# Performance work log

Measured on AMD Instinct MI355X. Metric: run time of the kernel, lower is better.

## Reference

```python
import jax, jax.numpy as jnp
import numpy as np

N = 20000      # total nodes across the mini-batch of graphs
E = 320000     # edges (avg degree 16)
B = 16         # graphs in the batch
HEADS = 8
EPS_BN = 1e-5
NEG_SLOPE = 0.2


def _lin(k, fan_in, fan_out):
    return (jax.random.normal(k, (fan_in, fan_out), jnp.float32) / np.float32(np.sqrt(fan_in)))


def setup_inputs() -> dict:
    key = jax.random.key(0)
    ks = jax.random.split(key, 24)
    inp = {}
    inp["x"] = jax.random.normal(ks[0], (N, 3), jnp.float32)
    inp["edge_index"] = jax.random.randint(ks[1], (2, E), 0, N, dtype=jnp.int32)
    inp["batch"] = jnp.sort(jax.random.randint(ks[2], (N,), 0, B, dtype=jnp.int32))
    # GATConv params: lin weight [in, heads*out], att_src/att_dst [heads,out], bias [heads*out]
    dims = [(3, 16), (128, 32), (256, 64)]
    for i, (cin, cout) in enumerate(dims, start=1):
        base = 3 + 5 * i
        inp[f"W{i}"] = _lin(ks[base], cin, HEADS * cout)
        inp[f"as{i}"] = jax.random.normal(ks[base + 1], (HEADS, cout), jnp.float32) * 0.1
        inp[f"ad{i}"] = jax.random.normal(ks[base + 2], (HEADS, cout), jnp.float32) * 0.1
        inp[f"b{i}"] = jnp.zeros((HEADS * cout,), jnp.float32)
        inp[f"g{i}"] = jnp.ones((HEADS * cout,), jnp.float32)
        inp[f"be{i}"] = jnp.zeros((HEADS * cout,), jnp.float32)
    inp["fcW"] = _lin(ks[20], 512, 10)
    inp["fcb"] = jnp.zeros((10,), jnp.float32)
    return inp


def gat_layer(x, src, dst, W, a_s, a_d, bias, heads, out_ch):
    n = x.shape[0]
    h = (x @ W).reshape(n, heads, out_ch)              # [N,H,C]
    al_s = jnp.einsum('nhc,hc->nh', h, a_s)            # [N,H]
    al_d = jnp.einsum('nhc,hc->nh', h, a_d)
    e = jax.nn.leaky_relu(al_s[src] + al_d[dst], NEG_SLOPE)   # [E,H]
    m = jax.ops.segment_max(e, dst, num_segments=n)    # per-dst softmax (stable)
    e = jnp.exp(e - m[dst])
    denom = jax.ops.segment_sum(e, dst, num_segments=n)
    alpha = e / (denom[dst] + 1e-16)
    out = jax.ops.segment_sum(h[src] * alpha[:, :, None], dst, num_segments=n)
    return out.reshape(n, heads * out_ch) + bias


def bn_relu(x, g, b):
    mu = x.mean(0)
    var = x.var(0)  # biased, as torch BN uses for normalization
    return jax.nn.relu((x - mu) * jax.lax.rsqrt(var + EPS_BN) * g + b)


def reference(x, edge_index, batch, W1, as1, ad1, b1, g1, be1,
              W2, as2, ad2, b2, g2, be2, W3, as3, ad3, b3, g3, be3, fcW, fcb):
    n = x.shape[0]
    loops = jnp.arange(n, dtype=edge_index.dtype)
    src = jnp.concatenate([edge_index[0], loops])  # add_self_loops=True (PyG default)
    dst = jnp.concatenate([edge_index[1], loops])
    h = bn_relu(gat_layer(x, src, dst, W1, as1, ad1, b1, HEADS, 16), g1, be1)
    h = bn_relu(gat_layer(h, src, dst, W2, as2, ad2, b2, HEADS, 32), g2, be2)
    h = bn_relu(gat_layer(h, src, dst, W3, as3, ad3, b3, HEADS, 64), g3, be3)
    pooled = jax.ops.segment_max(h, batch, num_segments=B)  # global_max_pool
    return pooled @ fcW + fcb
```

## Files before the change

### kernel.cpp

```cpp
#include <hip/hip_runtime.h>
#include <hip/hip_bf16.h>

#define HEADS 8
#define EPS_BN 1e-5f
#define NEG_SLOPE 0.2f
#define BN_NB 256

typedef __attribute__((ext_vector_type(8))) short bf16x8;
typedef __attribute__((ext_vector_type(4))) float f32x4;

__device__ __forceinline__ float bf2f(unsigned short u) {
    return __uint_as_float(((unsigned int)u) << 16);
}

__device__ __forceinline__ unsigned short f2bf(float f) {
    __hip_bfloat16 b = __float2bfloat16(f);
    return *reinterpret_cast<unsigned short*>(&b);
}

__device__ __forceinline__ void gld_lds16(const ushort* g, ushort* l) {
    __builtin_amdgcn_global_load_lds(
        (const __attribute__((address_space(1))) unsigned int*)g,
        (__attribute__((address_space(3))) unsigned int*)l, 16, 0, 0);
}


__global__ void count_kernel(const int* __restrict__ ei, int E, int N, int* __restrict__ counts) {
    int i = blockIdx.x * blockDim.x + threadIdx.x;
    int total = E + N;
    if (i >= total) return;
    int d = (i < E) ? ei[E + i] : (i - E);
    atomicAdd(&counts[d], 1);
}

__global__ __launch_bounds__(1024) void scan_block_kernel(const int* __restrict__ counts,
                                                          int* __restrict__ offs,
                                                          int* __restrict__ part, int n) {
    __shared__ int tile[1024];
    int tid = threadIdx.x;
    int gid = blockIdx.x * 1024 + tid;
    int v = (gid < n) ? counts[gid] : 0;
    tile[tid] = v;
    __syncthreads();
    for (int off = 1; off < 1024; off <<= 1) {
        int t = (tid >= off) ? tile[tid - off] : 0;
        __syncthreads();
        tile[tid] += t;
        __syncthreads();
    }
    if (gid < n) offs[gid + 1] = tile[tid];
    if (tid == 1023) part[blockIdx.x] = tile[1023];
}

__global__ __launch_bounds__(1024) void scan_add_kernel(int* __restrict__ offs,
                                                        const int* __restrict__ part, int n) {
    __shared__ int base;
    if (threadIdx.x == 0) {
        int s = 0;
        for (int i = 0; i < (int)blockIdx.x; ++i) s += part[i];
        base = s;
    }
    __syncthreads();
    int gid = blockIdx.x * 1024 + threadIdx.x;
    if (gid < n) offs[gid + 1] += base;
    if (gid == 0) offs[0] = 0;
}

__global__ void scatter_kernel(const int* __restrict__ ei, int E, int N,
                               const int* __restrict__ offs, int* __restrict__ cursor,
                               int* __restrict__ csr_src) {
    int i = blockIdx.x * blockDim.x + threadIdx.x;
    int total = E + N;
    if (i >= total) return;
    int s, d;
    if (i < E) { s = ei[i]; d = ei[E + i]; } else { s = i - E; d = i - E; }
    int slot = atomicAdd(&cursor[d], 1);
    csr_src[offs[d] + slot] = s;
}


__global__ __launch_bounds__(256) void linear1_al_kernel(const float* __restrict__ x,
                                                         const float* __restrict__ W,
                                                         const float* __restrict__ a_s,
                                                         const float* __restrict__ a_d,
                                                         ushort* __restrict__ h,
                                                         float* __restrict__ als,
                                                         float* __restrict__ ald, int N) {
    int tid = threadIdx.x;
    int n = blockIdx.x * 2 + (tid >> 7);
    int f = tid & 127;
    if (n >= N) return;
    float acc = x[n * 3 + 0] * W[f] + x[n * 3 + 1] * W[128 + f] + x[n * 3 + 2] * W[256 + f];
    h[(size_t)n * 128 + f] = f2bf(acc);
    float s = acc * a_s[f];
    float ds = acc * a_d[f];
    s += __shfl_xor(s, 1);  ds += __shfl_xor(ds, 1);
    s += __shfl_xor(s, 2);  ds += __shfl_xor(ds, 2);
    s += __shfl_xor(s, 4);  ds += __shfl_xor(ds, 4);
    s += __shfl_xor(s, 8);  ds += __shfl_xor(ds, 8);
    if ((f & 15) == 0) {
        int head = f >> 4;
        als[n * 8 + head] = s;
        ald[n * 8 + head] = ds;
    }
}


__global__ __launch_bounds__(256) void transpose_both_kernel(const float* __restrict__ W2,
                                                             ushort* __restrict__ Wt2,
                                                             const float* __restrict__ W3,
                                                             ushort* __restrict__ Wt3) {
    __shared__ float t[32][33];
    int bid = blockIdx.x;
    const float* W; ushort* Wt; int K, Nc, b;
    if (bid < 32) { W = W2; Wt = Wt2; K = 128; Nc = 256; b = bid; }
    else          { W = W3; Wt = Wt3; K = 256; Nc = 512; b = bid - 32; }
    int nb = Nc / 32;
    int bx = b % nb, by = b / nb;
    int n0 = bx * 32, k0 = by * 32;
    int lx = threadIdx.x & 31, ly = threadIdx.x >> 5;
    for (int r = ly; r < 32; r += 8) t[r][lx] = W[(size_t)(k0 + r) * Nc + n0 + lx];
    __syncthreads();
    for (int r = ly; r < 32; r += 8) Wt[(size_t)(n0 + r) * K + k0 + lx] = f2bf(t[lx][r]);
}


template<int F>
__global__ void prep_kernel(const float4* __restrict__ x, const float* __restrict__ scale,
                            const float* __restrict__ shift, ushort4* __restrict__ A, int n4) {
    int i = blockIdx.x * blockDim.x + threadIdx.x;
    if (i >= n4) return;
    float4 v = x[i];
    int f = (i << 2) & (F - 1);
    float4 sc = *(const float4*)(scale + f);
    float4 sh = *(const float4*)(shift + f);
    ushort4 u;
    u.x = f2bf(fmaxf(v.x * sc.x + sh.x, 0.f));
    u.y = f2bf(fmaxf(v.y * sc.y + sh.y, 0.f));
    u.z = f2bf(fmaxf(v.z * sc.z + sh.z, 0.f));
    u.w = f2bf(fmaxf(v.w * sc.w + sh.w, 0.f));
    A[i] = u;
}


template<int K, int C>
__global__ __launch_bounds__(256) void mfma_gemm_kernel(const ushort* __restrict__ A,
                                                        const ushort* __restrict__ Bt,
                                                        ushort* __restrict__ Cout,
                                                        const float* __restrict__ a_s,
                                                        const float* __restrict__ a_d,
                                                        float* __restrict__ als,
                                                        float* __restrict__ ald,
                                                        int M, int Ncols) {
    __shared__ __align__(16) ushort lA[128 * 64];
    __shared__ __align__(16) ushort lB[128 * 64];
    int tid = threadIdx.x;
    int l = tid & 63, w = tid >> 6;
    int m0 = blockIdx.x * 128;
    int n0 = blockIdx.y * 128;
    int wm = w >> 1, wn = w & 1;
    f32x4 zero = {0.f, 0.f, 0.f, 0.f};
    f32x4 acc[4][4];
#pragma unroll
    for (int m = 0; m < 4; ++m)
#pragma unroll
        for (int n = 0; n < 4; ++n) acc[m][n] = zero;

#pragma unroll
    for (int k0 = 0; k0 < K; k0 += 64) {
        if (k0) __syncthreads();
#pragma unroll
        for (int i = 0; i < 4; ++i) {
            int idx = (w * 4 + i) * 64 + l;
            int row = idx >> 3, p = idx & 7;
            int gc = (p ^ (row & 7)) * 8;
            int ar = m0 + row; ar = (ar < M) ? ar : (M - 1);
            gld_lds16(A + (size_t)ar * K + k0 + gc, &lA[idx * 8]);
            gld_lds16(Bt + (size_t)(n0 + row) * K + k0 + gc, &lB[idx * 8]);
        }
        __syncthreads();
#pragma unroll
        for (int ks = 0; ks < 2; ++ks) {
            bf16x8 af[4], bfr[4];
#pragma unroll
            for (int m = 0; m < 4; ++m) {
                int row = wm * 64 + m * 16 + (l & 15);
                int cp = (ks * 4 + (l >> 4)) ^ (row & 7);
                af[m] = *(const bf16x8*)&lA[row * 64 + cp * 8];
            }
#pragma unroll
            for (int n = 0; n < 4; ++n) {
                int row = wn * 64 + n * 16 + (l & 15);
                int cp = (ks * 4 + (l >> 4)) ^ (row & 7);
                bfr[n] = *(const bf16x8*)&lB[row * 64 + cp * 8];
            }
#pragma unroll
            for (int m = 0; m < 4; ++m)
#pragma unroll
                for (int n = 0; n < 4; ++n)
                    acc[m][n] = __builtin_amdgcn_mfma_f32_16x16x32_bf16(af[m], bfr[n], acc[m][n], 0, 0, 0);
        }
    }
    int lr = (l >> 4) * 4, lc = l & 15;
#pragma unroll
    for (int m = 0; m < 4; ++m) {
#pragma unroll
        for (int q = 0; q < 4; ++q) {
            int r = m0 + wm * 64 + m * 16 + lr + q;
            if (r < M) {
#pragma unroll
                for (int n = 0; n < 4; ++n) {
                    int c = n0 + wn * 64 + n * 16 + lc;
                    Cout[(size_t)r * Ncols + c] = f2bf(acc[m][n][q]);
                }
            }
        }
    }
    constexpr int GRP = (C == 64) ? 4 : 2;
    constexpr int NGRP = 4 / GRP;
    float asv[4], adv[4];
#pragma unroll
    for (int n = 0; n < 4; ++n) {
        int cc = n0 + wn * 64 + n * 16 + lc;
        asv[n] = a_s[cc];
        adv[n] = a_d[cc];
    }
#pragma unroll
    for (int m = 0; m < 4; ++m) {
#pragma unroll
        for (int q = 0; q < 4; ++q) {
            int r = m0 + wm * 64 + m * 16 + lr + q;
#pragma unroll
            for (int gg = 0; gg < NGRP; ++gg) {
                float s = 0.f, ds = 0.f;
#pragma unroll
                for (int nn = 0; nn < GRP; ++nn) {
                    int n = gg * GRP + nn;
                    s += acc[m][n][q] * asv[n];
                    ds += acc[m][n][q] * adv[n];
                }
                s += __shfl_xor(s, 1);  ds += __shfl_xor(ds, 1);
                s += __shfl_xor(s, 2);  ds += __shfl_xor(ds, 2);
                s += __shfl_xor(s, 4);  ds += __shfl_xor(ds, 4);
                s += __shfl_xor(s, 8);  ds += __shfl_xor(ds, 8);
                if (lc == 0 && r < M) {
                    int head = (n0 + wn * 64 + gg * (GRP * 16)) / C;
                    als[r * 8 + head] = s;
                    ald[r * 8 + head] = ds;
                }
            }
        }
    }
}


template<int CPL>
__device__ __forceinline__ void gather_accum(const ushort* hp, float wt, float* acc) {
    unsigned int u[CPL / 2];
    if constexpr (CPL == 8) {
        uint4 v = *(const uint4*)hp; u[0] = v.x; u[1] = v.y; u[2] = v.z; u[3] = v.w;
    } else if constexpr (CPL == 4) {
        uint2 v = *(const uint2*)hp; u[0] = v.x; u[1] = v.y;
    } else {
        u[0] = *(const unsigned int*)hp;
    }
#pragma unroll
    for (int j = 0; j < CPL / 2; ++j) {
        acc[2 * j]     += wt * __uint_as_float(u[j] << 16);
        acc[2 * j + 1] += wt * __uint_as_float(u[j] & 0xffff0000u);
    }
}

template<int F, int C>
__global__ __launch_bounds__(256) void aggregate_kernel(const ushort* __restrict__ h,
                                                        const float* __restrict__ als,
                                                        const float* __restrict__ ald,
                                                        const int* __restrict__ offs,
                                                        const int* __restrict__ csr_src,
                                                        const float* __restrict__ bias,
                                                        float* __restrict__ out, int N) {
    constexpr int CPL = F / 64;
    int w = threadIdx.x >> 6, l = threadIdx.x & 63;
    int d = blockIdx.x * 4 + w;
    if (d >= N) return;
    int start = offs[d];
    int deg = offs[d + 1] - start;
    int hf = l >> 3;
    int hw = l & 7;
    int jslot = l >> 3;
    float aldw = ald[d * 8 + hw];

    float m = -1e30f;
    for (int eb = 0; eb < deg; eb += 8) {
        int sE = 0;
        if (l < 8 && eb + l < deg) sE = csr_src[start + eb + l];
        int sj = __shfl(sE, jslot);
        if (eb + jslot < deg) {
            float v = als[sj * 8 + hw] + aldw;
            v = (v > 0.f) ? v : NEG_SLOPE * v;
            m = fmaxf(m, v);
        }
    }
    m = fmaxf(m, __shfl_xor(m, 8));
    m = fmaxf(m, __shfl_xor(m, 16));
    m = fmaxf(m, __shfl_xor(m, 32));

    float acc[CPL];
#pragma unroll
    for (int j = 0; j < CPL; ++j) acc[j] = 0.f;
    float dsum = 0.f;
    int nfull = deg & ~7;
    for (int eb = 0; eb < nfull; eb += 8) {
        int sE = (l < 8) ? csr_src[start + eb + l] : 0;
        int smy = __shfl(sE, jslot);
        float v = als[smy * 8 + hw] + aldw;
        v = (v > 0.f) ? v : NEG_SLOPE * v;
        float pw = __expf(v - m);
        dsum += pw;
#pragma unroll
        for (int j = 0; j < 8; ++j) {
            int sj = __shfl(sE, j);
            float wt = __shfl(pw, (j << 3) + hf);
            gather_accum<CPL>(h + (size_t)sj * F + l * CPL, wt, acc);
        }
    }
    int rem = deg - nfull;
    if (rem) {
        int sE = (l < rem) ? csr_src[start + nfull + l] : 0;
        int smy = __shfl(sE, jslot);
        float pw = 0.f;
        if (jslot < rem) {
            float v = als[smy * 8 + hw] + aldw;
            v = (v > 0.f) ? v : NEG_SLOPE * v;
            pw = __expf(v - m);
        }
        dsum += pw;
        for (int j = 0; j < rem; ++j) {
            int sj = __shfl(sE, j);
            float wt = __shfl(pw, (j << 3) + hf);
            gather_accum<CPL>(h + (size_t)sj * F + l * CPL, wt, acc);
        }
    }
    dsum += __shfl_xor(dsum, 8);
    dsum += __shfl_xor(dsum, 16);
    dsum += __shfl_xor(dsum, 32);
    float den = __shfl(dsum, hf);
    float inv = 1.0f / (den + 1e-16f);
    int cbase = l * CPL;
#pragma unroll
    for (int j = 0; j < CPL; ++j)
        out[(size_t)d * F + cbase + j] = acc[j] * inv + bias[cbase + j];
}


template<int F>
__global__ __launch_bounds__(256) void bnA_kernel(const float4* __restrict__ x4,
                                                  float* __restrict__ part,
                                                  int N, int npb) {
    constexpr int F4 = F / 4;
    constexpr int RPI = 256 / F4;
    __shared__ float sdata[256 * 8];
    int tid = threadIdx.x;
    int c4 = tid % F4;
    int ro = tid / F4;
    int n0 = blockIdx.x * npb;
    int n1 = n0 + npb;
    if (n1 > N) n1 = N;
    float s0 = 0, s1 = 0, s2 = 0, s3 = 0, q0 = 0, q1 = 0, q2 = 0, q3 = 0;
    for (int r = n0 + ro; r < n1; r += RPI) {
        float4 v = x4[(size_t)r * F4 + c4];
        s0 += v.x; s1 += v.y; s2 += v.z; s3 += v.w;
        q0 += v.x * v.x; q1 += v.y * v.y; q2 += v.z * v.z; q3 += v.w * v.w;
    }
    float* sp = &sdata[tid * 8];
    sp[0] = s0; sp[1] = s1; sp[2] = s2; sp[3] = s3;
    sp[4] = q0; sp[5] = q1; sp[6] = q2; sp[7] = q3;
    __syncthreads();
    if (tid < F4) {
        float t[8];
#pragma unroll
        for (int k = 0; k < 8; ++k) t[k] = sdata[tid * 8 + k];
        for (int j = 1; j < RPI; ++j) {
            const float* op = &sdata[(j * F4 + tid) * 8];
#pragma unroll
            for (int k = 0; k < 8; ++k) t[k] += op[k];
        }
        float* pb = part + (size_t)blockIdx.x * 2 * F;
#pragma unroll
        for (int k = 0; k < 4; ++k) {
            pb[tid * 4 + k]     = t[k];
            pb[F + tid * 4 + k] = t[4 + k];
        }
    }
}

template<int F>
__global__ void bnB_kernel(const float* __restrict__ part,
                           const float* __restrict__ g, const float* __restrict__ be,
                           float* __restrict__ scale, float* __restrict__ shift, int N) {
    int f = blockIdx.x * blockDim.x + threadIdx.x;
    if (f >= F) return;
    float sum = 0.f, sq = 0.f;
#pragma unroll 4
    for (int j = 0; j < BN_NB; ++j) {
        sum += part[(size_t)j * 2 * F + f];
        sq  += part[(size_t)j * 2 * F + F + f];
    }
    float invN = 1.0f / (float)N;
    float mean = sum * invN;
    float var = sq * invN - mean * mean;
    float sc = g[f] * rsqrtf(var + EPS_BN);
    scale[f] = sc;
    shift[f] = be[f] - mean * sc;
}


__global__ __launch_bounds__(256) void poolA_kernel(const float4* __restrict__ x4,
                                                    const int* __restrict__ batch,
                                                    const float* __restrict__ scale,
                                                    const float* __restrict__ shift,
                                                    float* __restrict__ pooled8, int N) {
    int tid = threadIdx.x;
    int c4 = tid & 127;
    int ro = tid >> 7;
    int n0 = blockIdx.x * 64;
    int n1 = n0 + 64;
    if (n1 > N) n1 = N;
    float4 sc = ((const float4*)scale)[c4];
    float4 sh = ((const float4*)shift)[c4];
    float* pbase = pooled8 + (size_t)(blockIdx.x & 7) * (16 * 512);
    float m0 = 0.f, m1 = 0.f, m2 = 0.f, m3 = 0.f;
    int cur = -1;
    for (int n = n0 + ro; n < n1; n += 2) {
        int b = batch[n];
        if (b != cur) {
            if (cur >= 0) {
                int base = cur * 512 + c4 * 4;
                atomicMax((int*)&pbase[base],     __float_as_int(m0));
                atomicMax((int*)&pbase[base + 1], __float_as_int(m1));
                atomicMax((int*)&pbase[base + 2], __float_as_int(m2));
                atomicMax((int*)&pbase[base + 3], __float_as_int(m3));
            }
            cur = b;
            m0 = m1 = m2 = m3 = 0.f;
        }
        float4 v = x4[(size_t)n * 128 + c4];
        m0 = fmaxf(m0, v.x * sc.x + sh.x);
        m1 = fmaxf(m1, v.y * sc.y + sh.y);
        m2 = fmaxf(m2, v.z * sc.z + sh.z);
        m3 = fmaxf(m3, v.w * sc.w + sh.w);
    }
    if (cur >= 0) {
        int base = cur * 512 + c4 * 4;
        atomicMax((int*)&pbase[base],     __float_as_int(m0));
        atomicMax((int*)&pbase[base + 1], __float_as_int(m1));
        atomicMax((int*)&pbase[base + 2], __float_as_int(m2));
        atomicMax((int*)&pbase[base + 3], __float_as_int(m3));
    }
}

__global__ __launch_bounds__(512) void poolFC_kernel(const float* __restrict__ pooled8,
                                                     const float* __restrict__ fcW,
                                                     const float* __restrict__ fcb,
                                                     float* __restrict__ out) {
    __shared__ float sp[16 * 513];
    __shared__ float sw[512 * 10];
    int tid = threadIdx.x;
    for (int c = tid; c < 16 * 512; c += 512) {
        float m = pooled8[c];
#pragma unroll
        for (int k = 1; k < 8; ++k) m = fmaxf(m, pooled8[k * 16 * 512 + c]);
        int b = c >> 9, f = c & 511;
        sp[b * 513 + f] = m;
    }
    for (int i = tid; i < 512 * 10; i += 512) sw[i] = fcW[i];
    __syncthreads();
    if (tid < 160) {
        int b = tid / 10, j = tid % 10;
        float acc = fcb[j];
        const float* spb = &sp[b * 513];
#pragma unroll 8
        for (int f = 0; f < 512; ++f) acc += spb[f] * sw[f * 10 + j];
        out[tid] = acc;
    }
}


extern "C" void kernel_launch(void* const* d_in, const int* in_sizes, int n_in,
                              void* d_out, int out_size, void* d_ws, size_t ws_size,
                              hipStream_t stream) {
    const float* x   = (const float*)d_in[0];
    const int* ei    = (const int*)d_in[1];
    const int* batch = (const int*)d_in[2];
    const float* W1  = (const float*)d_in[3];
    const float* as1 = (const float*)d_in[4];
    const float* ad1 = (const float*)d_in[5];
    const float* b1  = (const float*)d_in[6];
    const float* g1  = (const float*)d_in[7];
    const float* be1 = (const float*)d_in[8];
    const float* W2  = (const float*)d_in[9];
    const float* as2 = (const float*)d_in[10];
    const float* ad2 = (const float*)d_in[11];
    const float* b2  = (const float*)d_in[12];
    const float* g2  = (const float*)d_in[13];
    const float* be2 = (const float*)d_in[14];
    const float* W3  = (const float*)d_in[15];
    const float* as3 = (const float*)d_in[16];
    const float* ad3 = (const float*)d_in[17];
    const float* b3  = (const float*)d_in[18];
    const float* g3  = (const float*)d_in[19];
    const float* be3 = (const float*)d_in[20];
    const float* fcW = (const float*)d_in[21];
    const float* fcb = (const float*)d_in[22];
    float* out = (float*)d_out;

    int N = in_sizes[0] / 3;
    int E = in_sizes[1] / 2;

    char* p = (char*)d_ws;
    auto alloc = [&](size_t bytes) {
        char* r = p;
        p += (bytes + 255) & ~(size_t)255;
        return r;
    };
    char* zbase   = p;
    int*   counts = (int*)alloc((size_t)N * 4);
    int*   cursor = (int*)alloc((size_t)N * 4);
    float* pooled8 = (float*)alloc(8 * 16 * 512 * 4);
    size_t zbytes = (size_t)(p - zbase);
    int*   offs   = (int*)alloc((size_t)(N + 1) * 4);
    int*   part   = (int*)alloc(64 * 4);
    int*   csr    = (int*)alloc((size_t)(E + N) * 4);
    ushort* h     = (ushort*)alloc((size_t)N * 512 * 2);
    float* agg    = (float*)alloc((size_t)N * 512 * 4);
    ushort* Wt2   = (ushort*)alloc(256 * 128 * 2);
    ushort* Wt3   = (ushort*)alloc(512 * 256 * 2);
    float* als    = (float*)alloc((size_t)N * 8 * 4);
    float* ald    = (float*)alloc((size_t)N * 8 * 4);
    float* bnpart = (float*)alloc((size_t)BN_NB * 1024 * 4);
    float* scale  = (float*)alloc(512 * 4);
    float* shift  = (float*)alloc(512 * 4);
    ushort* Abuf  = (ushort*)(agg + (size_t)N * 256);

    int total_e = E + N;
    int nchunks = (N + 1023) / 1024;
    int mtiles = (N + 127) / 128;
    int bnnpb = (N + BN_NB - 1) / BN_NB;
    int ablocks = (N + 3) / 4;
    int pblocks = (N + 63) / 64;

    hipMemsetAsync(zbase, 0, zbytes, stream);

    count_kernel<<<(total_e + 255) / 256, 256, 0, stream>>>(ei, E, N, counts);
    scan_block_kernel<<<nchunks, 1024, 0, stream>>>(counts, offs, part, N);
    scan_add_kernel<<<nchunks, 1024, 0, stream>>>(offs, part, N);
    scatter_kernel<<<(total_e + 255) / 256, 256, 0, stream>>>(ei, E, N, offs, cursor, csr);

    transpose_both_kernel<<<160, 256, 0, stream>>>(W2, Wt2, W3, Wt3);

    linear1_al_kernel<<<(N + 1) / 2, 256, 0, stream>>>(x, W1, as1, ad1, h, als, ald, N);
    aggregate_kernel<128, 16><<<ablocks, 256, 0, stream>>>(h, als, ald, offs, csr, b1, agg, N);
    bnA_kernel<128><<<BN_NB, 256, 0, stream>>>((const float4*)agg, bnpart, N, bnnpb);
    bnB_kernel<128><<<1, 128, 0, stream>>>(bnpart, g1, be1, scale, shift, N);

    prep_kernel<128><<<(N * 128 / 4 + 255) / 256, 256, 0, stream>>>(
        (const float4*)agg, scale, shift, (ushort4*)Abuf, N * 128 / 4);
    mfma_gemm_kernel<128, 32><<<dim3(mtiles, 2), 256, 0, stream>>>(
        Abuf, Wt2, h, as2, ad2, als, ald, N, 256);
    aggregate_kernel<256, 32><<<ablocks, 256, 0, stream>>>(h, als, ald, offs, csr, b2, agg, N);
    bnA_kernel<256><<<BN_NB, 256, 0, stream>>>((const float4*)agg, bnpart, N, bnnpb);
    bnB_kernel<256><<<1, 256, 0, stream>>>(bnpart, g2, be2, scale, shift, N);

    prep_kernel<256><<<(N * 256 / 4 + 255) / 256, 256, 0, stream>>>(
        (const float4*)agg, scale, shift, (ushort4*)Abuf, N * 256 / 4);
    mfma_gemm_kernel<256, 64><<<dim3(mtiles, 4), 256, 0, stream>>>(
        Abuf, Wt3, h, as3, ad3, als, ald, N, 512);
    aggregate_kernel<512, 64><<<ablocks, 256, 0, stream>>>(h, als, ald, offs, csr, b3, agg, N);
    bnA_kernel<512><<<BN_NB, 256, 0, stream>>>((const float4*)agg, bnpart, N, bnnpb);
    bnB_kernel<512><<<2, 256, 0, stream>>>(bnpart, g3, be3, scale, shift, N);

    poolA_kernel<<<pblocks, 256, 0, stream>>>((const float4*)agg, batch, scale, shift, pooled8, N);
    poolFC_kernel<<<1, 512, 0, stream>>>(pooled8, fcW, fcb, out);
}
```

Measured before the change: 338.2 us.

## Store aggregation output in bf16 and use online softmax in aggregate

```diff
diff --git a/kernel.cpp b/kernel.cpp
--- a/kernel.cpp
+++ b/kernel.cpp
@@ -126,20 +126,20 @@
 
 
 template<int F>
-__global__ void prep_kernel(const float4* __restrict__ x, const float* __restrict__ scale,
+__global__ void prep_kernel(const ushort4* __restrict__ xb, const float* __restrict__ scale,
                             const float* __restrict__ shift, ushort4* __restrict__ A, int n4) {
     int i = blockIdx.x * blockDim.x + threadIdx.x;
     if (i >= n4) return;
-    float4 v = x[i];
+    ushort4 u = xb[i];
     int f = (i << 2) & (F - 1);
     float4 sc = *(const float4*)(scale + f);
     float4 sh = *(const float4*)(shift + f);
-    ushort4 u;
-    u.x = f2bf(fmaxf(v.x * sc.x + sh.x, 0.f));
-    u.y = f2bf(fmaxf(v.y * sc.y + sh.y, 0.f));
-    u.z = f2bf(fmaxf(v.z * sc.z + sh.z, 0.f));
-    u.w = f2bf(fmaxf(v.w * sc.w + sh.w, 0.f));
-    A[i] = u;
+    ushort4 o;
+    o.x = f2bf(fmaxf(bf2f(u.x) * sc.x + sh.x, 0.f));
+    o.y = f2bf(fmaxf(bf2f(u.y) * sc.y + sh.y, 0.f));
+    o.z = f2bf(fmaxf(bf2f(u.z) * sc.z + sh.z, 0.f));
+    o.w = f2bf(fmaxf(bf2f(u.w) * sc.w + sh.w, 0.f));
+    A[i] = o;
 }
 
 
@@ -278,7 +278,7 @@
                                                         const int* __restrict__ offs,
                                                         const int* __restrict__ csr_src,
                                                         const float* __restrict__ bias,
-                                                        float* __restrict__ out, int N) {
+                                                        ushort* __restrict__ outbf, int N) {
     constexpr int CPL = F / 64;
     int w = threadIdx.x >> 6, l = threadIdx.x & 63;
     int d = blockIdx.x * 4 + w;
@@ -290,33 +290,30 @@
     int jslot = l >> 3;
     float aldw = ald[d * 8 + hw];
 
-    float m = -1e30f;
-    for (int eb = 0; eb < deg; eb += 8) {
-        int sE = 0;
-        if (l < 8 && eb + l < deg) sE = csr_src[start + eb + l];
-        int sj = __shfl(sE, jslot);
-        if (eb + jslot < deg) {
-            float v = als[sj * 8 + hw] + aldw;
-            v = (v > 0.f) ? v : NEG_SLOPE * v;
-            m = fmaxf(m, v);
-        }
-    }
-    m = fmaxf(m, __shfl_xor(m, 8));
-    m = fmaxf(m, __shfl_xor(m, 16));
-    m = fmaxf(m, __shfl_xor(m, 32));
-
     float acc[CPL];
 #pragma unroll
     for (int j = 0; j < CPL; ++j) acc[j] = 0.f;
     float dsum = 0.f;
+    float mrun = -1e30f;
+
     int nfull = deg & ~7;
     for (int eb = 0; eb < nfull; eb += 8) {
         int sE = (l < 8) ? csr_src[start + eb + l] : 0;
         int smy = __shfl(sE, jslot);
         float v = als[smy * 8 + hw] + aldw;
         v = (v > 0.f) ? v : NEG_SLOPE * v;
-        float pw = __expf(v - m);
-        dsum += pw;
+        float bm = v;
+        bm = fmaxf(bm, __shfl_xor(bm, 8));
+        bm = fmaxf(bm, __shfl_xor(bm, 16));
+        bm = fmaxf(bm, __shfl_xor(bm, 32));
+        float mnew = fmaxf(mrun, bm);
+        float rs = __expf(mrun - mnew);
+        float pw = __expf(v - mnew);
+        dsum = dsum * rs + pw;
+        float rsg = __shfl(rs, hf);
+#pragma unroll
+        for (int j = 0; j < CPL; ++j) acc[j] *= rsg;
+        mrun = mnew;
 #pragma unroll
         for (int j = 0; j < 8; ++j) {
             int sj = __shfl(sE, j);
@@ -328,13 +325,22 @@
     if (rem) {
         int sE = (l < rem) ? csr_src[start + nfull + l] : 0;
         int smy = __shfl(sE, jslot);
-        float pw = 0.f;
+        float v = -1e30f;
         if (jslot < rem) {
-            float v = als[smy * 8 + hw] + aldw;
+            v = als[smy * 8 + hw] + aldw;
             v = (v > 0.f) ? v : NEG_SLOPE * v;
-            pw = __expf(v - m);
-        }
-        dsum += pw;
+        }
+        float bm = v;
+        bm = fmaxf(bm, __shfl_xor(bm, 8));
+        bm = fmaxf(bm, __shfl_xor(bm, 16));
+        bm = fmaxf(bm, __shfl_xor(bm, 32));
+        float mnew = fmaxf(mrun, bm);
+        float rs = __expf(mrun - mnew);
+        float pw = __expf(v - mnew);
+        dsum = dsum * rs + pw;
+        float rsg = __shfl(rs, hf);
+#pragma unroll
+        for (int j = 0; j < CPL; ++j) acc[j] *= rsg;
         for (int j = 0; j < rem; ++j) {
             int sj = __shfl(sE, j);
             float wt = __shfl(pw, (j << 3) + hf);
@@ -349,12 +355,12 @@
     int cbase = l * CPL;
 #pragma unroll
     for (int j = 0; j < CPL; ++j)
-        out[(size_t)d * F + cbase + j] = acc[j] * inv + bias[cbase + j];
+        outbf[(size_t)d * F + cbase + j] = f2bf(acc[j] * inv + bias[cbase + j]);
 }
 
 
 template<int F>
-__global__ __launch_bounds__(256) void bnA_kernel(const float4* __restrict__ x4,
+__global__ __launch_bounds__(256) void bnA_kernel(const ushort* __restrict__ xb,
                                                   float* __restrict__ part,
                                                   int N, int npb) {
     constexpr int F4 = F / 4;
@@ -368,9 +374,10 @@
     if (n1 > N) n1 = N;
     float s0 = 0, s1 = 0, s2 = 0, s3 = 0, q0 = 0, q1 = 0, q2 = 0, q3 = 0;
     for (int r = n0 + ro; r < n1; r += RPI) {
-        float4 v = x4[(size_t)r * F4 + c4];
-        s0 += v.x; s1 += v.y; s2 += v.z; s3 += v.w;
-        q0 += v.x * v.x; q1 += v.y * v.y; q2 += v.z * v.z; q3 += v.w * v.w;
+        ushort4 u = *(const ushort4*)(xb + (size_t)r * F + c4 * 4);
+        float v0 = bf2f(u.x), v1 = bf2f(u.y), v2 = bf2f(u.z), v3 = bf2f(u.w);
+        s0 += v0; s1 += v1; s2 += v2; s3 += v3;
+        q0 += v0 * v0; q1 += v1 * v1; q2 += v2 * v2; q3 += v3 * v3;
     }
     float* sp = &sdata[tid * 8];
     sp[0] = s0; sp[1] = s1; sp[2] = s2; sp[3] = s3;
@@ -415,7 +422,7 @@
 }
 
 
-__global__ __launch_bounds__(256) void poolA_kernel(const float4* __restrict__ x4,
+__global__ __launch_bounds__(256) void poolA_kernel(const ushort* __restrict__ xb,
                                                     const int* __restrict__ batch,
                                                     const float* __restrict__ scale,
                                                     const float* __restrict__ shift,
@@ -444,11 +451,11 @@
             cur = b;
             m0 = m1 = m2 = m3 = 0.f;
         }
-        float4 v = x4[(size_t)n * 128 + c4];
-        m0 = fmaxf(m0, v.x * sc.x + sh.x);
-        m1 = fmaxf(m1, v.y * sc.y + sh.y);
-        m2 = fmaxf(m2, v.z * sc.z + sh.z);
-        m3 = fmaxf(m3, v.w * sc.w + sh.w);
+        ushort4 u = *(const ushort4*)(xb + (size_t)n * 512 + c4 * 4);
+        m0 = fmaxf(m0, bf2f(u.x) * sc.x + sh.x);
+        m1 = fmaxf(m1, bf2f(u.y) * sc.y + sh.y);
+        m2 = fmaxf(m2, bf2f(u.z) * sc.z + sh.z);
+        m3 = fmaxf(m3, bf2f(u.w) * sc.w + sh.w);
     }
     if (cur >= 0) {
         int base = cur * 512 + c4 * 4;
@@ -532,7 +539,8 @@
     int*   part   = (int*)alloc(64 * 4);
     int*   csr    = (int*)alloc((size_t)(E + N) * 4);
     ushort* h     = (ushort*)alloc((size_t)N * 512 * 2);
-    float* agg    = (float*)alloc((size_t)N * 512 * 4);
+    ushort* aggbf = (ushort*)alloc((size_t)N * 512 * 2);
+    ushort* Abuf  = (ushort*)alloc((size_t)N * 512 * 2);
     ushort* Wt2   = (ushort*)alloc(256 * 128 * 2);
     ushort* Wt3   = (ushort*)alloc(512 * 256 * 2);
     float* als    = (float*)alloc((size_t)N * 8 * 4);
@@ -540,7 +548,6 @@
     float* bnpart = (float*)alloc((size_t)BN_NB * 1024 * 4);
     float* scale  = (float*)alloc(512 * 4);
     float* shift  = (float*)alloc(512 * 4);
-    ushort* Abuf  = (ushort*)(agg + (size_t)N * 256);
 
     int total_e = E + N;
     int nchunks = (N + 1023) / 1024;
@@ -559,26 +566,26 @@
     transpose_both_kernel<<<160, 256, 0, stream>>>(W2, Wt2, W3, Wt3);
 
     linear1_al_kernel<<<(N + 1) / 2, 256, 0, stream>>>(x, W1, as1, ad1, h, als, ald, N);
-    aggregate_kernel<128, 16><<<ablocks, 256, 0, stream>>>(h, als, ald, offs, csr, b1, agg, N);
-    bnA_kernel<128><<<BN_NB, 256, 0, stream>>>((const float4*)agg, bnpart, N, bnnpb);
+    aggregate_kernel<128, 16><<<ablocks, 256, 0, stream>>>(h, als, ald, offs, csr, b1, aggbf, N);
+    bnA_kernel<128><<<BN_NB, 256, 0, stream>>>(aggbf, bnpart, N, bnnpb);
     bnB_kernel<128><<<1, 128, 0, stream>>>(bnpart, g1, be1, scale, shift, N);
 
     prep_kernel<128><<<(N * 128 / 4 + 255) / 256, 256, 0, stream>>>(
-        (const float4*)agg, scale, shift, (ushort4*)Abuf, N * 128 / 4);
+        (const ushort4*)aggbf, scale, shift, (ushort4*)Abuf, N * 128 / 4);
     mfma_gemm_kernel<128, 32><<<dim3(mtiles, 2), 256, 0, stream>>>(
         Abuf, Wt2, h, as2, ad2, als, ald, N, 256);
-    aggregate_kernel<256, 32><<<ablocks, 256, 0, stream>>>(h, als, ald, offs, csr, b2, agg, N);
-    bnA_kernel<256><<<BN_NB, 256, 0, stream>>>((const float4*)agg, bnpart, N, bnnpb);
+    aggregate_kernel<256, 32><<<ablocks, 256, 0, stream>>>(h, als, ald, offs, csr, b2, aggbf, N);
+    bnA_kernel<256><<<BN_NB, 256, 0, stream>>>(aggbf, bnpart, N, bnnpb);
     bnB_kernel<256><<<1, 256, 0, stream>>>(bnpart, g2, be2, scale, shift, N);
 
     prep_kernel<256><<<(N * 256 / 4 + 255) / 256, 256, 0, stream>>>(
-        (const float4*)agg, scale, shift, (ushort4*)Abuf, N * 256 / 4);
+        (const ushort4*)aggbf, scale, shift, (ushort4*)Abuf, N * 256 / 4);
     mfma_gemm_kernel<256, 64><<<dim3(mtiles, 4), 256, 0, stream>>>(
         Abuf, Wt3, h, as3, ad3, als, ald, N, 512);
-    aggregate_kernel<512, 64><<<ablocks, 256, 0, stream>>>(h, als, ald, offs, csr, b3, agg, N);
-    bnA_kernel<512><<<BN_NB, 256, 0, stream>>>((const float4*)agg, bnpart, N, bnnpb);
+    aggregate_kernel<512, 64><<<ablocks, 256, 0, stream>>>(h, als, ald, offs, csr, b3, aggbf, N);
+    bnA_kernel<512><<<BN_NB, 256, 0, stream>>>(aggbf, bnpart, N, bnnpb);
     bnB_kernel<512><<<2, 256, 0, stream>>>(bnpart, g3, be3, scale, shift, N);
 
-    poolA_kernel<<<pblocks, 256, 0, stream>>>((const float4*)agg, batch, scale, shift, pooled8, N);
+    poolA_kernel<<<pblocks, 256, 0, stream>>>(aggbf, batch, scale, shift, pooled8, N);
     poolFC_kernel<<<1, 512, 0, stream>>>(pooled8, fcW, fcb, out);
 }
```

New measurement: 325.3 us. -3.8%, faster.
